# Kernel tuning notes

Hardware: AMD Instinct MI355X
Metric: run time of the kernel (lower is better)

The kernel has to match this reference:

```python
import jax, jax.numpy as jnp
import numpy as np

MARGIN = 0.2  # from init_kwargs
N, D, N_CLASSES = 8192, 256, 64


def setup_inputs() -> dict:
    key = jax.random.key(0)
    k1, k2 = jax.random.split(key)
    embeddings = jax.random.normal(k1, (N, D), dtype=jnp.float32)
    targets = jax.random.randint(k2, (N,), 0, N_CLASSES, dtype=jnp.int64)
    return {"embeddings": embeddings, "targets": targets}


def _mine_triplets(embeddings, targets):
    sq = jnp.sum(embeddings * embeddings, axis=1)  # [N]
    dist = -2.0 * (embeddings @ embeddings.T) + sq[None, :] + sq[:, None]  # [N, N]
    pos_mask = targets[:, None] == targets[None, :]  # same label (incl. self, as in original)
    NEG_INF = jnp.asarray(-1e30, dist.dtype)
    POS_INF = jnp.asarray(1e30, dist.dtype)
    hardest_pos = jnp.argmax(jnp.where(pos_mask, dist, NEG_INF), axis=1)  # [N]
    hardest_neg = jnp.argmin(jnp.where(pos_mask, POS_INF, dist), axis=1)  # [N]
    anchors = jnp.arange(targets.shape[0])
    return jnp.stack([anchors, hardest_pos, hardest_neg], axis=1)  # [N, 3]


def reference(embeddings, targets):
    triplets = _mine_triplets(embeddings, targets)
    a, p, n = triplets[:, 0], triplets[:, 1], triplets[:, 2]
    ap = jnp.sum((embeddings[a] - embeddings[p]) ** 2, axis=1)
    an = jnp.sum((embeddings[a] - embeddings[n]) ** 2, axis=1)
    losses = jax.nn.relu(ap - an + MARGIN)
    return losses.mean(), triplets
```

## Files before the change

kernel.cpp:

```cpp
#include <hip/hip_runtime.h>

#define NROWS 8192
#define DDIM 256
#define MARGIN_F 0.2f
#define CSPLIT 32

typedef _Float16 half8 __attribute__((ext_vector_type(8)));
typedef float f32x4 __attribute__((ext_vector_type(4)));
typedef float f32x16 __attribute__((ext_vector_type(16)));
typedef int i32x4 __attribute__((ext_vector_type(4)));

__device__ __forceinline__ void gld16(const void* g, void* l) {
  __builtin_amdgcn_global_load_lds(
      (const __attribute__((address_space(1))) void*)g,
      (__attribute__((address_space(3))) void*)l, 16, 0, 0);
}

__global__ __launch_bounds__(256)
void prep_kernel(const float* __restrict__ E, _Float16* __restrict__ Eh,
                 _Float16* __restrict__ El, float* __restrict__ sq) {
  __shared__ float scratch[256];
  const int t = threadIdx.x;
  const int r = t & 31;
  const int kseg = t >> 5;
  const int rg = blockIdx.x;
  const int row = rg * 32 + r;
  const float* src = &E[row * DDIM + kseg * 32];
  float s = 0.f;
#pragma unroll
  for (int sub = 0; sub < 4; ++sub) {
    const float4 f0 = *(const float4*)(src + sub * 8);
    const float4 f1 = *(const float4*)(src + sub * 8 + 4);
    const float v[8] = {f0.x, f0.y, f0.z, f0.w, f1.x, f1.y, f1.z, f1.w};
    half8 H, L;
#pragma unroll
    for (int e = 0; e < 8; ++e) {
      s = fmaf(v[e], v[e], s);
      const _Float16 hi = (_Float16)v[e];
      H[e] = hi;
      L[e] = (_Float16)(v[e] - (float)hi);
    }
    const int k0 = kseg * 32 + sub * 8;
    const int kt = k0 >> 4;
    const int g = (k0 >> 3) & 1;
    const int dst = (rg * 16 + kt) * 512 + g * 256 + r * 8;
    *(half8*)&Eh[dst] = H;
    *(half8*)&El[dst] = L;
  }
  scratch[t] = s;
  __syncthreads();
  if (t < 32) {
    float acc = 0.f;
#pragma unroll
    for (int seg = 0; seg < 8; ++seg) acc += scratch[seg * 32 + t];
    sq[rg * 32 + t] = acc;
  }
}

__global__ __launch_bounds__(512, 2)
void mine_kernel(const _Float16* __restrict__ Eh, const _Float16* __restrict__ El,
                 const int* __restrict__ T, const float* __restrict__ sq,
                 float* __restrict__ pv, int* __restrict__ pi,
                 float* __restrict__ nv, int* __restrict__ ni) {
  __shared__ __align__(16) _Float16 S[2][4][8192];

  const int tid = threadIdx.x;
  const int lane = tid & 63;
  const int w = tid >> 6;
  const int wi = w >> 1, wj = w & 1;
  const int l31 = lane & 31;
  const int rowbase = blockIdx.y * 256;
  const int colbase = blockIdx.x * 256;

  const int arr = w >> 1;
  const int shalf = w & 1;
  const _Float16* sA = (arr & 1) ? El : Eh;
  const int rgb = ((arr < 2) ? blockIdx.y : blockIdx.x) * 8;

  float sqi[2]; int ti[2];
#pragma unroll
  for (int fi = 0; fi < 2; ++fi) {
    const int i = rowbase + wi * 64 + fi * 32 + l31;
    sqi[fi] = sq[i];
    ti[fi] = T[i];
  }

  float bpv[2], bnv[2]; int bpi[2], bni[2];
#pragma unroll
  for (int fi = 0; fi < 2; ++fi) { bpv[fi] = -3e38f; bnv[fi] = 3e38f; bpi[fi] = 0; bni[fi] = 0; }

  f32x16 acc[4][2];
#pragma unroll
  for (int jf = 0; jf < 4; ++jf)
#pragma unroll
    for (int fi = 0; fi < 2; ++fi) acc[jf][fi] = (f32x16)(0.f);

#pragma unroll
  for (int c = 0; c < 8; ++c)
    gld16(sA + ((rgb + shalf * 4 + (c >> 1)) * 16 + (c & 1)) * 512 + lane * 8,
          &S[0][arr][((shalf * 4 + (c >> 1)) * 2 + (c & 1)) * 512]);
  __syncthreads();

  for (int ktg = 0; ktg < 8; ++ktg) {
    const int cur = ktg & 1;
#pragma unroll
    for (int p = 0; p < 2; ++p) {
      if (ktg < 7) {
#pragma unroll
        for (int cc = 0; cc < 4; ++cc) {
          const int c = p * 4 + cc;
          gld16(sA + ((rgb + shalf * 4 + (c >> 1)) * 16 + (ktg + 1) * 2 + (c & 1)) * 512 + lane * 8,
                &S[cur ^ 1][arr][((shalf * 4 + (c >> 1)) * 2 + (c & 1)) * 512]);
        }
      }
      half8 ajh[4], ajl[4];
#pragma unroll
      for (int jf = 0; jf < 4; ++jf) {
        const int o = ((wj * 4 + jf) * 2 + p) * 512 + lane * 8;
        ajh[jf] = *(const half8*)&S[cur][2][o];
        ajl[jf] = *(const half8*)&S[cur][3][o];
      }
      half8 bh[2], bl[2];
#pragma unroll
      for (int fi = 0; fi < 2; ++fi) {
        const int o = ((wi * 2 + fi) * 2 + p) * 512 + lane * 8;
        bh[fi] = *(const half8*)&S[cur][0][o];
        bl[fi] = *(const half8*)&S[cur][1][o];
      }
      __builtin_amdgcn_s_barrier();
      __builtin_amdgcn_s_setprio(1);
#pragma unroll
      for (int fi = 0; fi < 2; ++fi)
#pragma unroll
        for (int jf = 0; jf < 4; ++jf) {
          acc[jf][fi] = __builtin_amdgcn_mfma_f32_32x32x16_f16(ajh[jf], bh[fi], acc[jf][fi], 0, 0, 0);
          acc[jf][fi] = __builtin_amdgcn_mfma_f32_32x32x16_f16(ajl[jf], bh[fi], acc[jf][fi], 0, 0, 0);
          acc[jf][fi] = __builtin_amdgcn_mfma_f32_32x32x16_f16(ajh[jf], bl[fi], acc[jf][fi], 0, 0, 0);
        }
      __builtin_amdgcn_s_setprio(0);
      __builtin_amdgcn_s_barrier();
    }
    __syncthreads();
  }

  const int lh4 = (lane >> 5) * 4;
#pragma unroll
  for (int jf = 0; jf < 4; ++jf) {
    const int jfbase = colbase + wj * 128 + jf * 32;
#pragma unroll
    for (int q = 0; q < 4; ++q) {
      const int jb = jfbase + 8 * q + lh4;
      const f32x4 sqj = *(const f32x4*)&sq[jb];
      const i32x4 tj = *(const i32x4*)&T[jb];
#pragma unroll
      for (int fi = 0; fi < 2; ++fi) {
#pragma unroll
        for (int rr = 0; rr < 4; ++rr) {
          const float dst = fmaf(-2.f, acc[jf][fi][q * 4 + rr], sqi[fi] + sqj[rr]);
          const int jidx = jb + rr;
          if (ti[fi] == tj[rr]) {
            if (dst > bpv[fi]) { bpv[fi] = dst; bpi[fi] = jidx; }
          } else {
            if (dst < bnv[fi]) { bnv[fi] = dst; bni[fi] = jidx; }
          }
        }
      }
    }
  }

#pragma unroll
  for (int fi = 0; fi < 2; ++fi) {
    const float ov = __shfl_xor(bpv[fi], 32, 64);
    const int oi = __shfl_xor(bpi[fi], 32, 64);
    if (ov > bpv[fi] || (ov == bpv[fi] && oi < bpi[fi])) { bpv[fi] = ov; bpi[fi] = oi; }
    const float on = __shfl_xor(bnv[fi], 32, 64);
    const int oni = __shfl_xor(bni[fi], 32, 64);
    if (on < bnv[fi] || (on == bnv[fi] && oni < bni[fi])) { bnv[fi] = on; bni[fi] = oni; }
  }

  __syncthreads();
  float4* scr = (float4*)&S[0][0][0];
  if (wj == 1 && lane < 32) {
#pragma unroll
    for (int fi = 0; fi < 2; ++fi)
      scr[wi * 64 + fi * 32 + l31] =
          make_float4(bpv[fi], __int_as_float(bpi[fi]), bnv[fi], __int_as_float(bni[fi]));
  }
  __syncthreads();
  if (wj == 0 && lane < 32) {
#pragma unroll
    for (int fi = 0; fi < 2; ++fi) {
      const float4 o = scr[wi * 64 + fi * 32 + l31];
      const int oi = __float_as_int(o.y), oni = __float_as_int(o.w);
      if (o.x > bpv[fi] || (o.x == bpv[fi] && oi < bpi[fi])) { bpv[fi] = o.x; bpi[fi] = oi; }
      if (o.z < bnv[fi] || (o.z == bnv[fi] && oni < bni[fi])) { bnv[fi] = o.z; bni[fi] = oni; }
      const int row = rowbase + wi * 64 + fi * 32 + l31;
      const int oidx = row * CSPLIT + blockIdx.x;
      pv[oidx] = bpv[fi]; pi[oidx] = bpi[fi]; nv[oidx] = bnv[fi]; ni[oidx] = bni[fi];
    }
  }
}

__global__ __launch_bounds__(256)
void finish_kernel(const float* __restrict__ E,
                   const float* __restrict__ pv, const int* __restrict__ pi,
                   const float* __restrict__ nv, const int* __restrict__ ni,
                   float* __restrict__ out, float* __restrict__ bl) {
  const int w = threadIdx.x >> 6, lane = threadIdx.x & 63;
  const int row = blockIdx.x * 4 + w;
  float Pv = -3e38f, Nv = 3e38f; int Pi = 0, Ni = 0;
#pragma unroll
  for (int s = 0; s < CSPLIT; ++s) {
    const float p = pv[row * CSPLIT + s]; const int px = pi[row * CSPLIT + s];
    if (p > Pv || (p == Pv && px < Pi)) { Pv = p; Pi = px; }
    const float n = nv[row * CSPLIT + s]; const int nx = ni[row * CSPLIT + s];
    if (n < Nv || (n == Nv && nx < Ni)) { Nv = n; Ni = nx; }
  }
  const float4 a = *(const float4*)&E[row * DDIM + lane * 4];
  const float4 p4 = *(const float4*)&E[Pi * DDIM + lane * 4];
  const float4 n4 = *(const float4*)&E[Ni * DDIM + lane * 4];
  float ap = (a.x - p4.x) * (a.x - p4.x) + (a.y - p4.y) * (a.y - p4.y)
           + (a.z - p4.z) * (a.z - p4.z) + (a.w - p4.w) * (a.w - p4.w);
  float an = (a.x - n4.x) * (a.x - n4.x) + (a.y - n4.y) * (a.y - n4.y)
           + (a.z - n4.z) * (a.z - n4.z) + (a.w - n4.w) * (a.w - n4.w);
#pragma unroll
  for (int o = 32; o > 0; o >>= 1) {
    ap += __shfl_down(ap, o, 64);
    an += __shfl_down(an, o, 64);
  }
  __shared__ float ls[4];
  if (lane == 0) {
    out[1 + row * 3 + 0] = (float)row;
    out[1 + row * 3 + 1] = (float)Pi;
    out[1 + row * 3 + 2] = (float)Ni;
    ls[w] = fmaxf(ap - an + MARGIN_F, 0.f);
  }
  __syncthreads();
  if (threadIdx.x == 0) bl[blockIdx.x] = (ls[0] + ls[1]) + (ls[2] + ls[3]);
}

__global__ __launch_bounds__(256)
void sum_kernel(const float* __restrict__ bl, float* __restrict__ out) {
  __shared__ float s[256];
  float t = 0.f;
#pragma unroll
  for (int r = 0; r < (NROWS / 4) / 256; ++r) t += bl[threadIdx.x + r * 256];
  s[threadIdx.x] = t;
  __syncthreads();
  for (int o = 128; o > 0; o >>= 1) {
    if (threadIdx.x < o) s[threadIdx.x] += s[threadIdx.x + o];
    __syncthreads();
  }
  if (threadIdx.x == 0) out[0] = s[0] * (1.f / NROWS);
}

extern "C" void kernel_launch(void* const* d_in, const int* in_sizes, int n_in,
                              void* d_out, int out_size, void* d_ws, size_t ws_size,
                              hipStream_t stream) {
  const float* E = (const float*)d_in[0];
  const int* T = (const int*)d_in[1];
  float* out = (float*)d_out;

  _Float16* Eh = (_Float16*)d_ws;
  _Float16* El = Eh + NROWS * DDIM;
  float* sq = (float*)(El + NROWS * DDIM);
  float* pv = sq + NROWS;
  int*   pi = (int*)(pv + NROWS * CSPLIT);
  float* nv = (float*)(pi + NROWS * CSPLIT);
  int*   ni = (int*)(nv + NROWS * CSPLIT);
  float* bl = (float*)(ni + NROWS * CSPLIT);

  prep_kernel<<<NROWS / 32, 256, 0, stream>>>(E, Eh, El, sq);
  mine_kernel<<<dim3(NROWS / 256, NROWS / 256), 512, 0, stream>>>(Eh, El, T, sq, pv, pi, nv, ni);
  finish_kernel<<<NROWS / 4, 256, 0, stream>>>(E, pv, pi, nv, ni, out, bl);
  sum_kernel<<<1, 256, 0, stream>>>(bl, out);
}
```

Baseline: 152.7 us.

## Use four waves per block with larger per-wave MFMA tiles and one barrier per k-step

```diff
diff --git a/kernel.cpp b/kernel.cpp
--- a/kernel.cpp
+++ b/kernel.cpp
@@ -57,7 +57,7 @@
   }
 }
 
-__global__ __launch_bounds__(512, 2)
+__global__ __launch_bounds__(256, 1)
 void mine_kernel(const _Float16* __restrict__ Eh, const _Float16* __restrict__ El,
                  const int* __restrict__ T, const float* __restrict__ sq,
                  float* __restrict__ pv, int* __restrict__ pi,
@@ -72,75 +72,69 @@
   const int rowbase = blockIdx.y * 256;
   const int colbase = blockIdx.x * 256;
 
-  const int arr = w >> 1;
-  const int shalf = w & 1;
-  const _Float16* sA = (arr & 1) ? El : Eh;
-  const int rgb = ((arr < 2) ? blockIdx.y : blockIdx.x) * 8;
-
-  float sqi[2]; int ti[2];
-#pragma unroll
-  for (int fi = 0; fi < 2; ++fi) {
-    const int i = rowbase + wi * 64 + fi * 32 + l31;
+  const _Float16* sA = (w & 1) ? El : Eh;
+  const int rgb = ((w < 2) ? blockIdx.y : blockIdx.x) * 8;
+
+  float sqi[4]; int ti[4];
+#pragma unroll
+  for (int fi = 0; fi < 4; ++fi) {
+    const int i = rowbase + wi * 128 + fi * 32 + l31;
     sqi[fi] = sq[i];
     ti[fi] = T[i];
   }
 
-  float bpv[2], bnv[2]; int bpi[2], bni[2];
-#pragma unroll
-  for (int fi = 0; fi < 2; ++fi) { bpv[fi] = -3e38f; bnv[fi] = 3e38f; bpi[fi] = 0; bni[fi] = 0; }
-
-  f32x16 acc[4][2];
+  float bpv[4], bnv[4]; int bpi[4], bni[4];
+#pragma unroll
+  for (int fi = 0; fi < 4; ++fi) { bpv[fi] = -3e38f; bnv[fi] = 3e38f; bpi[fi] = 0; bni[fi] = 0; }
+
+  f32x16 acc[4][4];
 #pragma unroll
   for (int jf = 0; jf < 4; ++jf)
 #pragma unroll
-    for (int fi = 0; fi < 2; ++fi) acc[jf][fi] = (f32x16)(0.f);
-
-#pragma unroll
-  for (int c = 0; c < 8; ++c)
-    gld16(sA + ((rgb + shalf * 4 + (c >> 1)) * 16 + (c & 1)) * 512 + lane * 8,
-          &S[0][arr][((shalf * 4 + (c >> 1)) * 2 + (c & 1)) * 512]);
-  __syncthreads();
+    for (int fi = 0; fi < 4; ++fi) acc[jf][fi] = (f32x16)(0.f);
+
+#pragma unroll
+  for (int c = 0; c < 16; ++c)
+    gld16(sA + ((rgb + (c >> 1)) * 16 + (c & 1)) * 512 + lane * 8, &S[0][w][c * 512]);
 
   for (int ktg = 0; ktg < 8; ++ktg) {
     const int cur = ktg & 1;
+    __syncthreads();
+    if (ktg < 7) {
+#pragma unroll
+      for (int c = 0; c < 16; ++c)
+        gld16(sA + ((rgb + (c >> 1)) * 16 + (ktg + 1) * 2 + (c & 1)) * 512 + lane * 8,
+              &S[cur ^ 1][w][c * 512]);
+    }
+    half8 ah[2][4], al[2][4], bh[2][4], bl[2][4];
 #pragma unroll
     for (int p = 0; p < 2; ++p) {
-      if (ktg < 7) {
-#pragma unroll
-        for (int cc = 0; cc < 4; ++cc) {
-          const int c = p * 4 + cc;
-          gld16(sA + ((rgb + shalf * 4 + (c >> 1)) * 16 + (ktg + 1) * 2 + (c & 1)) * 512 + lane * 8,
-                &S[cur ^ 1][arr][((shalf * 4 + (c >> 1)) * 2 + (c & 1)) * 512]);
-        }
-      }
-      half8 ajh[4], ajl[4];
 #pragma unroll
       for (int jf = 0; jf < 4; ++jf) {
         const int o = ((wj * 4 + jf) * 2 + p) * 512 + lane * 8;
-        ajh[jf] = *(const half8*)&S[cur][2][o];
-        ajl[jf] = *(const half8*)&S[cur][3][o];
+        ah[p][jf] = *(const half8*)&S[cur][2][o];
+        al[p][jf] = *(const half8*)&S[cur][3][o];
       }
-      half8 bh[2], bl[2];
-#pragma unroll
-      for (int fi = 0; fi < 2; ++fi) {
-        const int o = ((wi * 2 + fi) * 2 + p) * 512 + lane * 8;
-        bh[fi] = *(const half8*)&S[cur][0][o];
-        bl[fi] = *(const half8*)&S[cur][1][o];
+#pragma unroll
+      for (int fi = 0; fi < 4; ++fi) {
+        const int o = ((wi * 4 + fi) * 2 + p) * 512 + lane * 8;
+        bh[p][fi] = *(const half8*)&S[cur][0][o];
+        bl[p][fi] = *(const half8*)&S[cur][1][o];
       }
-      __builtin_amdgcn_s_barrier();
+    }
+#pragma unroll
+    for (int p = 0; p < 2; ++p) {
       __builtin_amdgcn_s_setprio(1);
 #pragma unroll
-      for (int fi = 0; fi < 2; ++fi)
+      for (int fi = 0; fi < 4; ++fi)
 #pragma unroll
         for (int jf = 0; jf < 4; ++jf) {
-          acc[jf][fi] = __builtin_amdgcn_mfma_f32_32x32x16_f16(ajh[jf], bh[fi], acc[jf][fi], 0, 0, 0);
-          acc[jf][fi] = __builtin_amdgcn_mfma_f32_32x32x16_f16(ajl[jf], bh[fi], acc[jf][fi], 0, 0, 0);
-          acc[jf][fi] = __builtin_amdgcn_mfma_f32_32x32x16_f16(ajh[jf], bl[fi], acc[jf][fi], 0, 0, 0);
+          acc[jf][fi] = __builtin_amdgcn_mfma_f32_32x32x16_f16(ah[p][jf], bh[p][fi], acc[jf][fi], 0, 0, 0);
+          acc[jf][fi] = __builtin_amdgcn_mfma_f32_32x32x16_f16(al[p][jf], bh[p][fi], acc[jf][fi], 0, 0, 0);
+          acc[jf][fi] = __builtin_amdgcn_mfma_f32_32x32x16_f16(ah[p][jf], bl[p][fi], acc[jf][fi], 0, 0, 0);
         }
       __builtin_amdgcn_s_setprio(0);
-      __builtin_amdgcn_s_barrier();
-    }
-    __syncthreads();
+    }
   }
 
   const int lh4 = (lane >> 5) * 4;
@@ -153,7 +147,7 @@
       const f32x4 sqj = *(const f32x4*)&sq[jb];
       const i32x4 tj = *(const i32x4*)&T[jb];
 #pragma unroll
-      for (int fi = 0; fi < 2; ++fi) {
+      for (int fi = 0; fi < 4; ++fi) {
 #pragma unroll
         for (int rr = 0; rr < 4; ++rr) {
           const float dst = fmaf(-2.f, acc[jf][fi][q * 4 + rr], sqi[fi] + sqj[rr]);
@@ -169,7 +163,7 @@
   }
 
 #pragma unroll
-  for (int fi = 0; fi < 2; ++fi) {
+  for (int fi = 0; fi < 4; ++fi) {
     const float ov = __shfl_xor(bpv[fi], 32, 64);
     const int oi = __shfl_xor(bpi[fi], 32, 64);
     if (ov > bpv[fi] || (ov == bpv[fi] && oi < bpi[fi])) { bpv[fi] = ov; bpi[fi] = oi; }
@@ -182,19 +176,19 @@
   float4* scr = (float4*)&S[0][0][0];
   if (wj == 1 && lane < 32) {
 #pragma unroll
-    for (int fi = 0; fi < 2; ++fi)
-      scr[wi * 64 + fi * 32 + l31] =
+    for (int fi = 0; fi < 4; ++fi)
+      scr[wi * 128 + fi * 32 + l31] =
           make_float4(bpv[fi], __int_as_float(bpi[fi]), bnv[fi], __int_as_float(bni[fi]));
   }
   __syncthreads();
   if (wj == 0 && lane < 32) {
 #pragma unroll
-    for (int fi = 0; fi < 2; ++fi) {
-      const float4 o = scr[wi * 64 + fi * 32 + l31];
+    for (int fi = 0; fi < 4; ++fi) {
+      const float4 o = scr[wi * 128 + fi * 32 + l31];
       const int oi = __float_as_int(o.y), oni = __float_as_int(o.w);
       if (o.x > bpv[fi] || (o.x == bpv[fi] && oi < bpi[fi])) { bpv[fi] = o.x; bpi[fi] = oi; }
       if (o.z < bnv[fi] || (o.z == bnv[fi] && oni < bni[fi])) { bnv[fi] = o.z; bni[fi] = oni; }
-      const int row = rowbase + wi * 64 + fi * 32 + l31;
+      const int row = rowbase + wi * 128 + fi * 32 + l31;
       const int oidx = row * CSPLIT + blockIdx.x;
       pv[oidx] = bpv[fi]; pi[oidx] = bpi[fi]; nv[oidx] = bnv[fi]; ni[oidx] = bni[fi];
     }
@@ -271,7 +265,7 @@
   float* bl = (float*)(ni + NROWS * CSPLIT);
 
   prep_kernel<<<NROWS / 32, 256, 0, stream>>>(E, Eh, El, sq);
-  mine_kernel<<<dim3(NROWS / 256, NROWS / 256), 512, 0, stream>>>(Eh, El, T, sq, pv, pi, nv, ni);
+  mine_kernel<<<dim3(NROWS / 256, NROWS / 256), 256, 0, stream>>>(Eh, El, T, sq, pv, pi, nv, ni);
   finish_kernel<<<NROWS / 4, 256, 0, stream>>>(E, pv, pi, nv, ni, out, bl);
   sum_kernel<<<1, 256, 0, stream>>>(bl, out);
 }
```

After: 187.6 us. 22.8% more time.
